# Performance work log

Measured on AMD Instinct MI355X. Metric: run time of the kernel, lower is better.

Reference implementation:

```python
import jax, jax.numpy as jnp
import numpy as np

NUM_EXPERTS = 8
HIDDEN = 2048
INTER = 1408
TOKENS = 2048
TOP_K = 2


def setup_inputs() -> dict:
    key = jax.random.key(0)
    k1, k2, k3, k4, k5, k6 = jax.random.split(key, 6)
    hidden_states = jax.random.normal(k1, (TOKENS, HIDDEN), dtype=jnp.float32)
    top_k_index = jax.random.randint(k2, (TOKENS, TOP_K), 0, NUM_EXPERTS)
    top_k_weights = jax.random.uniform(k3, (TOKENS, TOP_K), dtype=jnp.float32)
    top_k_weights = top_k_weights / top_k_weights.sum(-1, keepdims=True)  # router-normalized
    scale = 0.02
    Wg = jax.random.normal(k4, (NUM_EXPERTS, INTER, HIDDEN), dtype=jnp.float32) * scale
    Wu = jax.random.normal(k5, (NUM_EXPERTS, INTER, HIDDEN), dtype=jnp.float32) * scale
    Wd = jax.random.normal(k6, (NUM_EXPERTS, HIDDEN, INTER), dtype=jnp.float32) * scale
    return {
        "hidden_states": hidden_states,
        "top_k_index": top_k_index,
        "top_k_weights": top_k_weights,
        "Wg": Wg,
        "Wu": Wu,
        "Wd": Wd,
    }


def reference(hidden_states, top_k_index, top_k_weights, Wg, Wu, Wd):
    # Combine weight per (token, expert): sum over top-k slots routed to that
    # expert (index_add in the original accumulates duplicate routes identically).
    E = Wg.shape[0]
    cw = (jax.nn.one_hot(top_k_index, E, dtype=hidden_states.dtype)
          * top_k_weights[..., None]).sum(axis=1)            # [T, E]
    # Per-expert SwiGLU MLP computed as grouped GEMMs over all tokens.
    gate = jnp.einsum('th,eih->tei', hidden_states, Wg)       # [T, E, I]
    up = jnp.einsum('th,eih->tei', hidden_states, Wu)         # [T, E, I]
    h = jax.nn.silu(gate) * up                                # [T, E, I]
    out_e = jnp.einsum('tei,ehi->teh', h, Wd)                 # [T, E, H]
    # Weighted combine: tokens not routed to an expert have cw == 0.
    return jnp.einsum('teh,te->th', out_e, cw)                # [T, H]
```

## Files before the change

kernel.cpp:

```cpp
#include <hip/hip_runtime.h>
#include <hip/hip_bf16.h>
#include <stdint.h>

#define TOKENS 2048
#define HIDDEN 2048
#define INTER  1408
#define NEXP   8
#define NPAIR  4096

typedef __attribute__((ext_vector_type(8))) short bf16x8;
typedef __attribute__((ext_vector_type(4))) float f32x4;

static __device__ __forceinline__ unsigned short f2b(float f) {
    union { float f; uint32_t u; } v; v.f = f;
    uint32_t r = (v.u + 0x7FFFu + ((v.u >> 16) & 1u)) >> 16;
    return (unsigned short)r;
}

#define GLDS(SRC, DST) \
    __builtin_amdgcn_global_load_lds( \
        (const __attribute__((address_space(1))) unsigned int*)(SRC), \
        (__attribute__((address_space(3))) unsigned int*)(DST), 16, 0, 0)

__global__ void route_k(const int* __restrict__ idx, const float* __restrict__ w,
                        int* __restrict__ off, int* __restrict__ tok,
                        float* __restrict__ wgt) {
    __shared__ int cnt[NEXP];
    __shared__ int cur[NEXP];
    int tid = threadIdx.x;
    if (tid < NEXP) cnt[tid] = 0;
    __syncthreads();
    for (int i = tid; i < NPAIR; i += 256) atomicAdd(&cnt[idx[i]], 1);
    __syncthreads();
    if (tid == 0) {
        int s = 0;
        for (int e = 0; e < NEXP; ++e) { off[e] = s; cur[e] = s; s += cnt[e]; }
        off[NEXP] = s;
    }
    __syncthreads();
    for (int i = tid; i < NPAIR; i += 256) {
        int e = idx[i];
        int p = atomicAdd(&cur[e], 1);
        tok[p] = i >> 1;
        wgt[p] = w[i];
    }
}

__global__ void conv_k(const float* __restrict__ x, unsigned short* __restrict__ xb, int n) {
    int i = (blockIdx.x * blockDim.x + threadIdx.x) * 4;
    if (i < n) {
        float4 v = *(const float4*)(x + i);
        ushort4 o;
        o.x = f2b(v.x); o.y = f2b(v.y); o.z = f2b(v.z); o.w = f2b(v.w);
        *(ushort4*)(xb + i) = o;
    }
}


__global__ __launch_bounds__(256, 4) void gemm1_k(
    const unsigned short* __restrict__ Xb,
    const unsigned short* __restrict__ Wgb, const unsigned short* __restrict__ Wub,
    const int* __restrict__ off, const int* __restrict__ tok,
    unsigned short* __restrict__ H) {

    const int e    = blockIdx.x;
    const int o0   = off[e];
    const int cnt  = off[e + 1] - o0;
    const int row0 = blockIdx.y * 128;
    if (row0 >= cnt) return;
    const int col0 = blockIdx.z * 64;

    __shared__ __align__(16) unsigned short sA[2][128 * 32];
    __shared__ __align__(16) unsigned short sG[2][64 * 32];
    __shared__ __align__(16) unsigned short sU[2][64 * 32];
    __shared__ int stok[128];

    const int tid = threadIdx.x;
    if (tid < 128) {
        int r = row0 + tid;
        stok[tid] = tok[o0 + (r < cnt ? r : cnt - 1)];
    }
    __syncthreads();

    int sa_[2]; const unsigned short* gA[2];
    #pragma unroll
    for (int j = 0; j < 2; ++j) {
        int s = tid + 256 * j, r = s >> 2, q = s & 3;
        sa_[j] = s * 8;
        gA[j] = Xb + (size_t)stok[r] * HIDDEN + ((q ^ ((r >> 1) & 3)) << 3);
    }
    int sb_; const unsigned short* gG; const unsigned short* gU;
    {
        int s = tid, r = s >> 2, q = s & 3;
        sb_ = s * 8;
        int c = (q ^ ((r >> 1) & 3)) << 3;
        gG = Wgb + ((size_t)e * INTER + col0 + r) * HIDDEN + c;
        gU = Wub + ((size_t)e * INTER + col0 + r) * HIDDEN + c;
    }

    const int wave = tid >> 6, lane = tid & 63;
    const int wm = (wave >> 1) * 64, wn = (wave & 1) * 32;
    const int lm = lane & 15, quad = lane >> 4;
    const int swz = ((quad ^ ((lane >> 1) & 3)) << 3);

    f32x4 accg[4][2], accu[4][2];
    #pragma unroll
    for (int i = 0; i < 4; ++i)
        #pragma unroll
        for (int j = 0; j < 2; ++j) {
            accg[i][j] = (f32x4){0.f, 0.f, 0.f, 0.f};
            accu[i][j] = (f32x4){0.f, 0.f, 0.f, 0.f};
        }

    GLDS(gA[0], &sA[0][sa_[0]]);
    GLDS(gA[1], &sA[0][sa_[1]]);
    GLDS(gG, &sG[0][sb_]);
    GLDS(gU, &sU[0][sb_]);
    __syncthreads();

    const int NS = HIDDEN / 32;
    for (int ks = 0; ks < NS; ++ks) {
        const int b = ks & 1;
        if (ks + 1 < NS) {
            const int ko = (ks + 1) * 32;
            GLDS(gA[0] + ko, &sA[b ^ 1][sa_[0]]);
            GLDS(gA[1] + ko, &sA[b ^ 1][sa_[1]]);
            GLDS(gG + ko, &sG[b ^ 1][sb_]);
            GLDS(gU + ko, &sU[b ^ 1][sb_]);
        }
        bf16x8 af[4], gf[2], uf[2];
        #pragma unroll
        for (int mi = 0; mi < 4; ++mi)
            af[mi] = *(const bf16x8*)&sA[b][(wm + mi * 16 + lm) * 32 + swz];
        #pragma unroll
        for (int ni = 0; ni < 2; ++ni) {
            gf[ni] = *(const bf16x8*)&sG[b][(wn + ni * 16 + lm) * 32 + swz];
            uf[ni] = *(const bf16x8*)&sU[b][(wn + ni * 16 + lm) * 32 + swz];
        }
        #pragma unroll
        for (int mi = 0; mi < 4; ++mi)
            #pragma unroll
            for (int ni = 0; ni < 2; ++ni) {
                accg[mi][ni] = __builtin_amdgcn_mfma_f32_16x16x32_bf16(af[mi], gf[ni], accg[mi][ni], 0, 0, 0);
                accu[mi][ni] = __builtin_amdgcn_mfma_f32_16x16x32_bf16(af[mi], uf[ni], accu[mi][ni], 0, 0, 0);
            }
        __syncthreads();
    }

    #pragma unroll
    for (int mi = 0; mi < 4; ++mi) {
        #pragma unroll
        for (int reg = 0; reg < 4; ++reg) {
            int lr = wm + mi * 16 + quad * 4 + reg;
            int r  = row0 + lr;
            if (r < cnt) {
                size_t hrow = (size_t)(o0 + r) * INTER;
                #pragma unroll
                for (int ni = 0; ni < 2; ++ni) {
                    float g = accg[mi][ni][reg];
                    float u = accu[mi][ni][reg];
                    float h = g / (1.f + __expf(-g)) * u;
                    H[hrow + col0 + wn + ni * 16 + lm] = f2b(h);
                }
            }
        }
    }
}

__global__ __launch_bounds__(256, 4) void gemm2_k(
    const unsigned short* __restrict__ H,
    const unsigned short* __restrict__ Wdb,
    const int* __restrict__ off, const int* __restrict__ tok,
    const float* __restrict__ wgt,
    float* __restrict__ out) {

    const int e    = blockIdx.x;
    const int o0   = off[e];
    const int cnt  = off[e + 1] - o0;
    const int row0 = blockIdx.y * 128;
    if (row0 >= cnt) return;
    const int col0 = blockIdx.z * 128;

    __shared__ __align__(16) unsigned short sA[2][128 * 32];
    __shared__ __align__(16) unsigned short sB[2][128 * 32];
    __shared__ int   stok[128];
    __shared__ float swgt[128];

    const int tid = threadIdx.x;
    if (tid < 128) {
        int r  = row0 + tid;
        int rr = (r < cnt ? r : cnt - 1);
        stok[tid] = tok[o0 + rr];
        swgt[tid] = wgt[o0 + rr];
    }
    __syncthreads();

    int sa_[2];
    const unsigned short* gA[2]; const unsigned short* gB[2];
    #pragma unroll
    for (int j = 0; j < 2; ++j) {
        int s = tid + 256 * j, r = s >> 2, q = s & 3;
        sa_[j] = s * 8;
        int c = (q ^ ((r >> 1) & 3)) << 3;
        int gr = row0 + r; if (gr >= cnt) gr = cnt - 1;
        gA[j] = H + (size_t)(o0 + gr) * INTER + c;
        gB[j] = Wdb + ((size_t)e * HIDDEN + col0 + r) * INTER + c;
    }

    const int wave = tid >> 6, lane = tid & 63;
    const int wm = (wave >> 1) * 64, wn = (wave & 1) * 64;
    const int lm = lane & 15, quad = lane >> 4;
    const int swz = ((quad ^ ((lane >> 1) & 3)) << 3);

    f32x4 acc[4][4];
    #pragma unroll
    for (int i = 0; i < 4; ++i)
        #pragma unroll
        for (int j = 0; j < 4; ++j) acc[i][j] = (f32x4){0.f, 0.f, 0.f, 0.f};

    #pragma unroll
    for (int j = 0; j < 2; ++j) {
        GLDS(gA[j], &sA[0][sa_[j]]);
        GLDS(gB[j], &sB[0][sa_[j]]);
    }
    __syncthreads();

    const int NS = INTER / 32;
    for (int ks = 0; ks < NS; ++ks) {
        const int b = ks & 1;
        if (ks + 1 < NS) {
            const int ko = (ks + 1) * 32;
            #pragma unroll
            for (int j = 0; j < 2; ++j) {
                GLDS(gA[j] + ko, &sA[b ^ 1][sa_[j]]);
                GLDS(gB[j] + ko, &sB[b ^ 1][sa_[j]]);
            }
        }
        bf16x8 af[4], bf[4];
        #pragma unroll
        for (int mi = 0; mi < 4; ++mi)
            af[mi] = *(const bf16x8*)&sA[b][(wm + mi * 16 + lm) * 32 + swz];
        #pragma unroll
        for (int ni = 0; ni < 4; ++ni)
            bf[ni] = *(const bf16x8*)&sB[b][(wn + ni * 16 + lm) * 32 + swz];
        #pragma unroll
        for (int mi = 0; mi < 4; ++mi)
            #pragma unroll
            for (int ni = 0; ni < 4; ++ni)
                acc[mi][ni] = __builtin_amdgcn_mfma_f32_16x16x32_bf16(af[mi], bf[ni], acc[mi][ni], 0, 0, 0);
        __syncthreads();
    }

    #pragma unroll
    for (int mi = 0; mi < 4; ++mi) {
        #pragma unroll
        for (int reg = 0; reg < 4; ++reg) {
            int lr = wm + mi * 16 + quad * 4 + reg;
            int r  = row0 + lr;
            if (r < cnt) {
                int   t = stok[lr];
                float w = swgt[lr];
                #pragma unroll
                for (int ni = 0; ni < 4; ++ni)
                    atomicAdd(&out[(size_t)t * HIDDEN + col0 + wn + ni * 16 + lm],
                              w * acc[mi][ni][reg]);
            }
        }
    }
}

extern "C" void kernel_launch(void* const* d_in, const int* in_sizes, int n_in,
                              void* d_out, int out_size, void* d_ws, size_t ws_size,
                              hipStream_t stream) {
    const float* X   = (const float*)d_in[0];
    const int*   idx = (const int*)d_in[1];
    const float* tw  = (const float*)d_in[2];
    const float* Wg  = (const float*)d_in[3];
    const float* Wu  = (const float*)d_in[4];
    const float* Wd  = (const float*)d_in[5];
    float* out = (float*)d_out;

    char* ws = (char*)d_ws;
    const size_t OFF_TOK = 64;
    const size_t OFF_WGT = 64 + (size_t)NPAIR * 4;
    const size_t OFF_XB  = 65536;
    const size_t OFF_H   = OFF_XB + (size_t)TOKENS * HIDDEN * 2;
    const size_t WELEMS  = (size_t)NEXP * INTER * HIDDEN;
    const size_t OFF_WG  = OFF_H + (size_t)NPAIR * INTER * 2;
    const size_t OFF_WU  = OFF_WG + WELEMS * 2;
    const size_t OFF_WD  = OFF_WU + WELEMS * 2;

    int*            off = (int*)ws;
    int*            tok = (int*)(ws + OFF_TOK);
    float*          wgt = (float*)(ws + OFF_WGT);
    unsigned short* Xb  = (unsigned short*)(ws + OFF_XB);
    unsigned short* H   = (unsigned short*)(ws + OFF_H);
    unsigned short* Wgb = (unsigned short*)(ws + OFF_WG);
    unsigned short* Wub = (unsigned short*)(ws + OFF_WU);
    unsigned short* Wdb = (unsigned short*)(ws + OFF_WD);

    hipMemsetAsync(d_out, 0, (size_t)out_size * sizeof(float), stream);

    route_k<<<1, 256, 0, stream>>>(idx, tw, off, tok, wgt);
    conv_k<<<(TOKENS * HIDDEN / 4 + 255) / 256, 256, 0, stream>>>(X, Xb, TOKENS * HIDDEN);

    const int wn4 = (int)(WELEMS / 4);
    conv_k<<<(wn4 + 255) / 256, 256, 0, stream>>>(Wg, Wgb, (int)WELEMS);
    conv_k<<<(wn4 + 255) / 256, 256, 0, stream>>>(Wu, Wub, (int)WELEMS);
    conv_k<<<(wn4 + 255) / 256, 256, 0, stream>>>(Wd, Wdb, (int)WELEMS);

    gemm1_k<<<dim3(NEXP, NPAIR / 128, INTER / 64), 256, 0, stream>>>(Xb, Wgb, Wub, off, tok, H);
    gemm2_k<<<dim3(NEXP, NPAIR / 128, HIDDEN / 128), 256, 0, stream>>>(H, Wdb, off, tok, wgt, out);
}
```

Before: 476.0 us.

## Triple-buffer LDS with partial vmcnt waits and single barrier per k-step

Both grouped GEMM kernels move from double to triple LDS buffering. Loads are issued two k-steps ahead, and each step waits with s_waitcnt vmcnt(4) so only the older stage has to land, followed by one s_barrier instead of two __syncthreads. The MFMA block is also bracketed with s_setprio to favour math waves. This should hide more global-load latency, at the cost of more LDS per block and a lower occupancy hint (launch bounds 4→3). The hand-written waitcnt also leans on the compiler not reordering the loads.

```diff
diff --git a/kernel.cpp b/kernel.cpp
--- a/kernel.cpp
+++ b/kernel.cpp
@@ -21,6 +21,10 @@
     __builtin_amdgcn_global_load_lds( \
         (const __attribute__((address_space(1))) unsigned int*)(SRC), \
         (__attribute__((address_space(3))) unsigned int*)(DST), 16, 0, 0)
+
+#define WAITVM4() asm volatile("s_waitcnt vmcnt(4)" ::: "memory")
+#define WAITVM0() asm volatile("s_waitcnt vmcnt(0)" ::: "memory")
+#define BARRIER() asm volatile("s_barrier" ::: "memory")
 
 __global__ void route_k(const int* __restrict__ idx, const float* __restrict__ w,
                         int* __restrict__ off, int* __restrict__ tok,
@@ -57,7 +61,7 @@
 }
 
 
-__global__ __launch_bounds__(256, 4) void gemm1_k(
+__global__ __launch_bounds__(256, 3) void gemm1_k(
     const unsigned short* __restrict__ Xb,
     const unsigned short* __restrict__ Wgb, const unsigned short* __restrict__ Wub,
     const int* __restrict__ off, const int* __restrict__ tok,
@@ -70,9 +74,9 @@
     if (row0 >= cnt) return;
     const int col0 = blockIdx.z * 64;
 
-    __shared__ __align__(16) unsigned short sA[2][128 * 32];
-    __shared__ __align__(16) unsigned short sG[2][64 * 32];
-    __shared__ __align__(16) unsigned short sU[2][64 * 32];
+    __shared__ __align__(16) unsigned short sA[3][128 * 32];
+    __shared__ __align__(16) unsigned short sG[3][64 * 32];
+    __shared__ __align__(16) unsigned short sU[3][64 * 32];
     __shared__ int stok[128];
 
     const int tid = threadIdx.x;
@@ -112,31 +116,37 @@
             accu[i][j] = (f32x4){0.f, 0.f, 0.f, 0.f};
         }
 
-    GLDS(gA[0], &sA[0][sa_[0]]);
-    GLDS(gA[1], &sA[0][sa_[1]]);
-    GLDS(gG, &sG[0][sb_]);
-    GLDS(gU, &sU[0][sb_]);
-    __syncthreads();
+    GLDS(gA[0],      &sA[0][sa_[0]]);
+    GLDS(gA[1],      &sA[0][sa_[1]]);
+    GLDS(gG,         &sG[0][sb_]);
+    GLDS(gU,         &sU[0][sb_]);
+    GLDS(gA[0] + 32, &sA[1][sa_[0]]);
+    GLDS(gA[1] + 32, &sA[1][sa_[1]]);
+    GLDS(gG + 32,    &sG[1][sb_]);
+    GLDS(gU + 32,    &sU[1][sb_]);
 
     const int NS = HIDDEN / 32;
+    int rb = 0, wb = 2;
     for (int ks = 0; ks < NS; ++ks) {
-        const int b = ks & 1;
-        if (ks + 1 < NS) {
-            const int ko = (ks + 1) * 32;
-            GLDS(gA[0] + ko, &sA[b ^ 1][sa_[0]]);
-            GLDS(gA[1] + ko, &sA[b ^ 1][sa_[1]]);
-            GLDS(gG + ko, &sG[b ^ 1][sb_]);
-            GLDS(gU + ko, &sU[b ^ 1][sb_]);
+        if (ks + 1 < NS) WAITVM4(); else WAITVM0();
+        BARRIER();
+        if (ks + 2 < NS) {
+            const int ko = (ks + 2) * 32;
+            GLDS(gA[0] + ko, &sA[wb][sa_[0]]);
+            GLDS(gA[1] + ko, &sA[wb][sa_[1]]);
+            GLDS(gG + ko,    &sG[wb][sb_]);
+            GLDS(gU + ko,    &sU[wb][sb_]);
         }
         bf16x8 af[4], gf[2], uf[2];
         #pragma unroll
         for (int mi = 0; mi < 4; ++mi)
-            af[mi] = *(const bf16x8*)&sA[b][(wm + mi * 16 + lm) * 32 + swz];
+            af[mi] = *(const bf16x8*)&sA[rb][(wm + mi * 16 + lm) * 32 + swz];
         #pragma unroll
         for (int ni = 0; ni < 2; ++ni) {
-            gf[ni] = *(const bf16x8*)&sG[b][(wn + ni * 16 + lm) * 32 + swz];
-            uf[ni] = *(const bf16x8*)&sU[b][(wn + ni * 16 + lm) * 32 + swz];
-        }
+            gf[ni] = *(const bf16x8*)&sG[rb][(wn + ni * 16 + lm) * 32 + swz];
+            uf[ni] = *(const bf16x8*)&sU[rb][(wn + ni * 16 + lm) * 32 + swz];
+        }
+        __builtin_amdgcn_s_setprio(1);
         #pragma unroll
         for (int mi = 0; mi < 4; ++mi)
             #pragma unroll
@@ -144,7 +154,9 @@
                 accg[mi][ni] = __builtin_amdgcn_mfma_f32_16x16x32_bf16(af[mi], gf[ni], accg[mi][ni], 0, 0, 0);
                 accu[mi][ni] = __builtin_amdgcn_mfma_f32_16x16x32_bf16(af[mi], uf[ni], accu[mi][ni], 0, 0, 0);
             }
-        __syncthreads();
+        __builtin_amdgcn_s_setprio(0);
+        rb = (rb == 2) ? 0 : rb + 1;
+        wb = (wb == 2) ? 0 : wb + 1;
     }
 
     #pragma unroll
@@ -167,7 +179,7 @@
     }
 }
 
-__global__ __launch_bounds__(256, 4) void gemm2_k(
+__global__ __launch_bounds__(256, 3) void gemm2_k(
     const unsigned short* __restrict__ H,
     const unsigned short* __restrict__ Wdb,
     const int* __restrict__ off, const int* __restrict__ tok,
@@ -181,8 +193,8 @@
     if (row0 >= cnt) return;
     const int col0 = blockIdx.z * 128;
 
-    __shared__ __align__(16) unsigned short sA[2][128 * 32];
-    __shared__ __align__(16) unsigned short sB[2][128 * 32];
+    __shared__ __align__(16) unsigned short sA[3][128 * 32];
+    __shared__ __align__(16) unsigned short sB[3][128 * 32];
     __shared__ int   stok[128];
     __shared__ float swgt[128];
 
@@ -220,35 +232,44 @@
 
     #pragma unroll
     for (int j = 0; j < 2; ++j) {
-        GLDS(gA[j], &sA[0][sa_[j]]);
-        GLDS(gB[j], &sB[0][sa_[j]]);
-    }
-    __syncthreads();
+        GLDS(gA[j],      &sA[0][sa_[j]]);
+        GLDS(gB[j],      &sB[0][sa_[j]]);
+    }
+    #pragma unroll
+    for (int j = 0; j < 2; ++j) {
+        GLDS(gA[j] + 32, &sA[1][sa_[j]]);
+        GLDS(gB[j] + 32, &sB[1][sa_[j]]);
+    }
 
     const int NS = INTER / 32;
+    int rb = 0, wb = 2;
     for (int ks = 0; ks < NS; ++ks) {
-        const int b = ks & 1;
-        if (ks + 1 < NS) {
-            const int ko = (ks + 1) * 32;
+        if (ks + 1 < NS) WAITVM4(); else WAITVM0();
+        BARRIER();
+        if (ks + 2 < NS) {
+            const int ko = (ks + 2) * 32;
             #pragma unroll
             for (int j = 0; j < 2; ++j) {
-                GLDS(gA[j] + ko, &sA[b ^ 1][sa_[j]]);
-                GLDS(gB[j] + ko, &sB[b ^ 1][sa_[j]]);
+                GLDS(gA[j] + ko, &sA[wb][sa_[j]]);
+                GLDS(gB[j] + ko, &sB[wb][sa_[j]]);
             }
         }
         bf16x8 af[4], bf[4];
         #pragma unroll
         for (int mi = 0; mi < 4; ++mi)
-            af[mi] = *(const bf16x8*)&sA[b][(wm + mi * 16 + lm) * 32 + swz];
+            af[mi] = *(const bf16x8*)&sA[rb][(wm + mi * 16 + lm) * 32 + swz];
         #pragma unroll
         for (int ni = 0; ni < 4; ++ni)
-            bf[ni] = *(const bf16x8*)&sB[b][(wn + ni * 16 + lm) * 32 + swz];
+            bf[ni] = *(const bf16x8*)&sB[rb][(wn + ni * 16 + lm) * 32 + swz];
+        __builtin_amdgcn_s_setprio(1);
         #pragma unroll
         for (int mi = 0; mi < 4; ++mi)
             #pragma unroll
             for (int ni = 0; ni < 4; ++ni)
                 acc[mi][ni] = __builtin_amdgcn_mfma_f32_16x16x32_bf16(af[mi], bf[ni], acc[mi][ni], 0, 0, 0);
-        __syncthreads();
+        __builtin_amdgcn_s_setprio(0);
+        rb = (rb == 2) ? 0 : rb + 1;
+        wb = (wb == 2) ? 0 : wb + 1;
     }
 
     #pragma unroll
```

After: 486.8 us. +2.3%, slower.

## Replace atomic scatter-add with per-pair output buffer and gather combine

Applied to the files above, without the earlier changes.

gemm2 now writes unweighted per-pair results to a workspace buffer with plain stores instead of atomically adding weighted results into the output. A new combine kernel gathers the two routed rows per token through an inverse permutation built in routing, applies the router weights, and writes the output. This removes the output memset and the atomics. The three weight conversion kernels are also merged into one grid-stride kernel. The trade-off is an extra 32MB fp32 temporary that is written and read back, plus one more launch.

```diff
diff --git a/kernel.cpp b/kernel.cpp
--- a/kernel.cpp
+++ b/kernel.cpp
@@ -22,9 +22,9 @@
         (const __attribute__((address_space(1))) unsigned int*)(SRC), \
         (__attribute__((address_space(3))) unsigned int*)(DST), 16, 0, 0)
 
-__global__ void route_k(const int* __restrict__ idx, const float* __restrict__ w,
+__global__ void route_k(const int* __restrict__ idx,
                         int* __restrict__ off, int* __restrict__ tok,
-                        float* __restrict__ wgt) {
+                        int* __restrict__ inv) {
     __shared__ int cnt[NEXP];
     __shared__ int cur[NEXP];
     int tid = threadIdx.x;
@@ -42,7 +42,7 @@
         int e = idx[i];
         int p = atomicAdd(&cur[e], 1);
         tok[p] = i >> 1;
-        wgt[p] = w[i];
+        inv[i] = p;
     }
 }
 
@@ -54,6 +54,43 @@
         o.x = f2b(v.x); o.y = f2b(v.y); o.z = f2b(v.z); o.w = f2b(v.w);
         *(ushort4*)(xb + i) = o;
     }
+}
+
+__global__ void conv3_k(const float* __restrict__ a, unsigned short* __restrict__ ab,
+                        const float* __restrict__ b, unsigned short* __restrict__ bb,
+                        const float* __restrict__ c, unsigned short* __restrict__ cb,
+                        int n4) {
+    int stride = gridDim.x * blockDim.x;
+    for (int i = blockIdx.x * blockDim.x + threadIdx.x; i < n4; i += stride) {
+        int j = i * 4;
+        float4 v = *(const float4*)(a + j);
+        ushort4 o;
+        o.x = f2b(v.x); o.y = f2b(v.y); o.z = f2b(v.z); o.w = f2b(v.w);
+        *(ushort4*)(ab + j) = o;
+        v = *(const float4*)(b + j);
+        o.x = f2b(v.x); o.y = f2b(v.y); o.z = f2b(v.z); o.w = f2b(v.w);
+        *(ushort4*)(bb + j) = o;
+        v = *(const float4*)(c + j);
+        o.x = f2b(v.x); o.y = f2b(v.y); o.z = f2b(v.z); o.w = f2b(v.w);
+        *(ushort4*)(cb + j) = o;
+    }
+}
+
+__global__ void combine_k(const float* __restrict__ tmp, const int* __restrict__ inv,
+                          const float* __restrict__ tw, float* __restrict__ out) {
+    int i = blockIdx.x * blockDim.x + threadIdx.x;
+    int t = i >> 9;
+    int c = (i & 511) * 4;
+    int p0 = inv[2 * t], p1 = inv[2 * t + 1];
+    float w0 = tw[2 * t], w1 = tw[2 * t + 1];
+    float4 x = *(const float4*)(tmp + (size_t)p0 * HIDDEN + c);
+    float4 y = *(const float4*)(tmp + (size_t)p1 * HIDDEN + c);
+    float4 o;
+    o.x = w0 * x.x + w1 * y.x;
+    o.y = w0 * x.y + w1 * y.y;
+    o.z = w0 * x.z + w1 * y.z;
+    o.w = w0 * x.w + w1 * y.w;
+    *(float4*)(out + (size_t)t * HIDDEN + c) = o;
 }
 
 
@@ -170,9 +207,8 @@
 __global__ __launch_bounds__(256, 4) void gemm2_k(
     const unsigned short* __restrict__ H,
     const unsigned short* __restrict__ Wdb,
-    const int* __restrict__ off, const int* __restrict__ tok,
-    const float* __restrict__ wgt,
-    float* __restrict__ out) {
+    const int* __restrict__ off,
+    float* __restrict__ tmp) {
 
     const int e    = blockIdx.x;
     const int o0   = off[e];
@@ -183,17 +219,8 @@
 
     __shared__ __align__(16) unsigned short sA[2][128 * 32];
     __shared__ __align__(16) unsigned short sB[2][128 * 32];
-    __shared__ int   stok[128];
-    __shared__ float swgt[128];
 
     const int tid = threadIdx.x;
-    if (tid < 128) {
-        int r  = row0 + tid;
-        int rr = (r < cnt ? r : cnt - 1);
-        stok[tid] = tok[o0 + rr];
-        swgt[tid] = wgt[o0 + rr];
-    }
-    __syncthreads();
 
     int sa_[2];
     const unsigned short* gA[2]; const unsigned short* gB[2];
@@ -258,12 +285,10 @@
             int lr = wm + mi * 16 + quad * 4 + reg;
             int r  = row0 + lr;
             if (r < cnt) {
-                int   t = stok[lr];
-                float w = swgt[lr];
+                size_t trow = (size_t)(o0 + r) * HIDDEN;
                 #pragma unroll
                 for (int ni = 0; ni < 4; ++ni)
-                    atomicAdd(&out[(size_t)t * HIDDEN + col0 + wn + ni * 16 + lm],
-                              w * acc[mi][ni][reg]);
+                    tmp[trow + col0 + wn + ni * 16 + lm] = acc[mi][ni][reg];
             }
         }
     }
@@ -282,33 +307,30 @@
 
     char* ws = (char*)d_ws;
     const size_t OFF_TOK = 64;
-    const size_t OFF_WGT = 64 + (size_t)NPAIR * 4;
+    const size_t OFF_INV = OFF_TOK + (size_t)NPAIR * 4;
     const size_t OFF_XB  = 65536;
     const size_t OFF_H   = OFF_XB + (size_t)TOKENS * HIDDEN * 2;
     const size_t WELEMS  = (size_t)NEXP * INTER * HIDDEN;
     const size_t OFF_WG  = OFF_H + (size_t)NPAIR * INTER * 2;
     const size_t OFF_WU  = OFF_WG + WELEMS * 2;
     const size_t OFF_WD  = OFF_WU + WELEMS * 2;
+    const size_t OFF_TMP = OFF_WD + WELEMS * 2;
 
     int*            off = (int*)ws;
     int*            tok = (int*)(ws + OFF_TOK);
-    float*          wgt = (float*)(ws + OFF_WGT);
+    int*            inv = (int*)(ws + OFF_INV);
     unsigned short* Xb  = (unsigned short*)(ws + OFF_XB);
     unsigned short* H   = (unsigned short*)(ws + OFF_H);
     unsigned short* Wgb = (unsigned short*)(ws + OFF_WG);
     unsigned short* Wub = (unsigned short*)(ws + OFF_WU);
     unsigned short* Wdb = (unsigned short*)(ws + OFF_WD);
-
-    hipMemsetAsync(d_out, 0, (size_t)out_size * sizeof(float), stream);
-
-    route_k<<<1, 256, 0, stream>>>(idx, tw, off, tok, wgt);
+    float*          tmp = (float*)(ws + OFF_TMP);
+
+    route_k<<<1, 256, 0, stream>>>(idx, off, tok, inv);
     conv_k<<<(TOKENS * HIDDEN / 4 + 255) / 256, 256, 0, stream>>>(X, Xb, TOKENS * HIDDEN);
-
-    const int wn4 = (int)(WELEMS / 4);
-    conv_k<<<(wn4 + 255) / 256, 256, 0, stream>>>(Wg, Wgb, (int)WELEMS);
-    conv_k<<<(wn4 + 255) / 256, 256, 0, stream>>>(Wu, Wub, (int)WELEMS);
-    conv_k<<<(wn4 + 255) / 256, 256, 0, stream>>>(Wd, Wdb, (int)WELEMS);
+    conv3_k<<<4096, 256, 0, stream>>>(Wg, Wgb, Wu, Wub, Wd, Wdb, (int)(WELEMS / 4));
 
     gemm1_k<<<dim3(NEXP, NPAIR / 128, INTER / 64), 256, 0, stream>>>(Xb, Wgb, Wub, off, tok, H);
-    gemm2_k<<<dim3(NEXP, NPAIR / 128, HIDDEN / 128), 256, 0, stream>>>(H, Wdb, off, tok, wgt, out);
-}
+    gemm2_k<<<dim3(NEXP, NPAIR / 128, HIDDEN / 128), 256, 0, stream>>>(H, Wdb, off, tmp);
+    combine_k<<<TOKENS * (HIDDEN / 4) / 256, 256, 0, stream>>>(tmp, inv, tw, out);
+}
```

Measured after the change: 492.6 us. 3.5% more time.
